# Kernel optimization log

Measured on AMD Instinct MI355X. Metric: run time of the kernel, lower is better.

## Reference

```python
import jax, jax.numpy as jnp
import numpy as np

B, A, F = 8192, 8, 256      # batch, n_agents, per-agent obs feature dim
NA = 16                     # n_actions per agent
H1, H2 = 1024, 1024
OBS_D = A * F               # 2048 flattened obs dim
ACT_D = A * NA              # 128 joint action dim
IN_D = OBS_D + ACT_D        # 2176 MLP input dim


def setup_inputs() -> dict:
    key = jax.random.key(0)
    ks = jax.random.split(key, 8)
    s = 0.02
    return {
        "obs": jax.random.normal(ks[0], (B, A, F), dtype=jnp.float32),
        "all_actions": jax.random.uniform(ks[1], (B, ACT_D), dtype=jnp.float32),
        # per-agent stacked MLP params (agent axis first)
        "W1": jax.random.normal(ks[2], (A, IN_D, H1), dtype=jnp.float32) * s,
        "b1": jnp.zeros((A, H1), dtype=jnp.float32),
        "W2": jax.random.normal(ks[3], (A, H1, H2), dtype=jnp.float32) * s,
        "b2": jnp.zeros((A, H2), dtype=jnp.float32),
        "W3": jax.random.normal(ks[4], (A, H2, NA), dtype=jnp.float32) * s,
        "b3": jnp.zeros((A, NA), dtype=jnp.float32),
    }


def reference(obs, all_actions, W1, b1, W2, b2, W3, b3):
    b_s = obs.shape[0]
    obs_flat = obs.reshape(b_s, OBS_D)                      # [B, A*F]
    # mask[a, g] = 0 on agent a's own action block, 1 elsewhere
    mask = 1.0 - jnp.repeat(jnp.eye(A, dtype=obs.dtype), NA, axis=1)  # [A, A*NA]
    # split W1 into obs / action columns (equivalent to concat-then-dense)
    W1o = W1[:, :OBS_D, :]                                  # [A, OBS_D, H1]
    W1a = W1[:, OBS_D:, :]                                  # [A, ACT_D, H1]
    h1 = jax.nn.relu(
        jnp.einsum("bd,adh->bah", obs_flat, W1o)
        + jnp.einsum("bg,ag,agh->bah", all_actions, mask, W1a)
        + b1
    )                                                        # [B, A, H1]
    h2 = jax.nn.relu(jnp.einsum("bah,ahk->bak", h1, W2) + b2)  # [B, A, H2]
    out = jnp.einsum("bak,akn->ban", h2, W3) + b3              # [B, A, NA]
    return out.reshape(b_s, A * NA)
```

## Files before the change

### kernel.cpp

```cpp
#include <hip/hip_runtime.h>
#include <hip/hip_bf16.h>
#include <cstdint>
#include <cstddef>

typedef __bf16 bf16;
typedef __attribute__((ext_vector_type(8))) __bf16 bf16x8;
typedef __attribute__((ext_vector_type(4))) float f32x4;
typedef __attribute__((ext_vector_type(4))) int i32x4;
typedef __attribute__((address_space(3))) const bf16* lds_cp;

#define B_SZ  8192
#define NAGENT 8
#define NA_N  16
#define OBS_DD 2048
#define ACT_DD 128
#define IN_DD 2176
#define H1_D  1024
#define H2_D  1024

#define BM 256
#define BN 256
#define BK 64
#define GRID_M (B_SZ / BM)
#define GRID_N (1024 / BN)

__device__ __forceinline__ void gload16(const void* g, void* l) {
    __builtin_amdgcn_global_load_lds(
        (__attribute__((address_space(1))) void*)(g),
        (__attribute__((address_space(3))) void*)(l), 16, 0, 0);
}

__global__ void k_prep(const float* __restrict__ obs, const float* __restrict__ act,
                       bf16* __restrict__ xb, const float* __restrict__ b3,
                       float* __restrict__ out, const float* __restrict__ W3,
                       bf16* __restrict__ w3t) {
    const int NX = B_SZ * (IN_DD / 8);
    const int NO = B_SZ * 128 / 4;
    const int NW3 = NAGENT * NA_N * H2_D;
    int idx = blockIdx.x * blockDim.x + threadIdx.x;
    if (idx < NX) {
        const int chunks = IN_DD / 8;
        int b = idx / chunks;
        int c8 = idx - b * chunks;
        const float* src = (c8 < OBS_DD / 8)
            ? (obs + (size_t)b * OBS_DD + c8 * 8)
            : (act + (size_t)b * ACT_DD + (c8 - OBS_DD / 8) * 8);
        float4 v0 = ((const float4*)src)[0];
        float4 v1 = ((const float4*)src)[1];
        bf16x8 o;
        o[0] = (bf16)v0.x; o[1] = (bf16)v0.y; o[2] = (bf16)v0.z; o[3] = (bf16)v0.w;
        o[4] = (bf16)v1.x; o[5] = (bf16)v1.y; o[6] = (bf16)v1.z; o[7] = (bf16)v1.w;
        ((bf16x8*)(xb + (size_t)b * IN_DD))[c8] = o;
    } else if (idx < NX + NO) {
        int i = idx - NX;
        int c = (i & 31) * 4;
        float4 v = make_float4(b3[c], b3[c + 1], b3[c + 2], b3[c + 3]);
        ((float4*)out)[i] = v;
    } else if (idx < NX + NO + NW3) {
        int i = idx - NX - NO;
        int a = i / (NA_N * H2_D);
        int n = (i / H2_D) % NA_N;
        int k = i % H2_D;
        w3t[i] = (bf16)W3[(size_t)a * H2_D * NAGENT * 0 + (size_t)a * H2_D * NA_N + (size_t)k * NA_N + n];
    }
}

__global__ void k_transpose_w12(const float* __restrict__ W1, bf16* __restrict__ W1T,
                                const float* __restrict__ W2, bf16* __restrict__ W2T) {
    __shared__ float tile[32][33];
    const int z = blockIdx.z;
    const bool isW1 = (z < 8);
    const int a = isW1 ? z : z - 8;
    const int K = isW1 ? IN_DD : H1_D;
    const int H = 1024;
    const int maskStart = isW1 ? OBS_DD : (1 << 30);
    if (!isW1 && blockIdx.x >= (H1_D / 32)) return;
    const float* s = (isW1 ? W1 : W2) + (size_t)a * K * H;
    bf16* d = (isW1 ? W1T : W2T) + (size_t)a * K * H;
    int k0 = blockIdx.x * 32, h0 = blockIdx.y * 32;
    int tx = threadIdx.x, ty = threadIdx.y;
    #pragma unroll
    for (int i = 0; i < 32; i += 8) {
        int k = k0 + ty + i;
        float v = s[(size_t)k * H + h0 + tx];
        if (k >= maskStart) {
            int g = k - maskStart;
            if ((g >> 4) == a) v = 0.f;
        }
        tile[ty + i][tx] = v;
    }
    __syncthreads();
    #pragma unroll
    for (int i = 0; i < 32; i += 8) {
        d[(size_t)(h0 + ty + i) * K + k0 + tx] = (bf16)tile[tx][ty + i];
    }
}

#define DSR4(d0, d1, d2, d3, addr, O0, O1, O2, O3)                      \
    asm volatile("ds_read_b128 %0, %4 offset:" #O0 "\n\t"               \
                 "ds_read_b128 %1, %4 offset:" #O1 "\n\t"               \
                 "ds_read_b128 %2, %4 offset:" #O2 "\n\t"               \
                 "ds_read_b128 %3, %4 offset:" #O3                      \
                 : "=&v"(d0), "=&v"(d1), "=&v"(d2), "=&v"(d3)           \
                 : "v"(addr))

#define BC(x) __builtin_bit_cast(bf16x8, x)

template<int FUSE>
__global__ __launch_bounds__(512, 1)
void k_gemm256(const bf16* __restrict__ Ain, size_t aStride, int lda,
               const bf16* __restrict__ Bw, const float* __restrict__ bias,
               bf16* __restrict__ Cout, size_t cStride, int K,
               int aOff, int gridZ,
               const bf16* __restrict__ W3Tp, float* __restrict__ outp) {
    extern __shared__ bf16 lds[];

    const int tid = threadIdx.x;
    const int w = tid >> 6;
    const int l = tid & 63;

    int flat = blockIdx.x + GRID_M * (blockIdx.y + GRID_N * blockIdx.z);
    int q8 = (GRID_M * GRID_N * gridZ) >> 3;
    int lin2 = (flat & 7) * q8 + (flat >> 3);
    const int mt = lin2 % GRID_M;
    int rest = lin2 / GRID_M;
    const int ntile = rest % GRID_N;
    const int az = rest / GRID_N;
    const int aw = az + aOff;

    const int rowBase = mt * BM;
    const int colBase = ntile * BN;
    const bf16* Aag = Ain + (size_t)az * aStride;
    const bf16* Bag = Bw + (size_t)aw * (size_t)1024 * K;

    const int wr = (w >> 2) * 128;
    const int wc = (w & 3) * 64;
    const int lr = l & 15;
    const int lq = l >> 4;

    const int rowA = (wr + lr) * BK;
    const int rowB = (wc + lr) * BK;
    const int ck0 = ((lq ^ (lr & 7)) * 8);
    const int ck1 = (((4 + lq) ^ (lr & 7)) * 8);

    const int sRow = w * 16 + (l >> 3);
    const int sCol = ((l & 7) ^ (l >> 3)) * 8;
    const bf16* pA0 = Aag + (size_t)(rowBase + sRow) * lda + sCol;
    const bf16* pA1 = Aag + (size_t)(rowBase + 128 + sRow) * lda + sCol;
    const bf16* pB0 = Bag + (size_t)(colBase + sRow) * K + sCol;
    const bf16* pB1 = Bag + (size_t)(colBase + 128 + sRow) * K + sCol;
    const size_t l8a = (size_t)8 * lda;
    const size_t l8b = (size_t)8 * K;

    const int nkt = K / BK;

#define STAGE_A(t1, half) do {                                              \
        const bf16* g_ = ((half) ? pA1 : pA0) + (t1) * BK;                  \
        bf16* d_ = &lds[(((t1) & 1) * 16384) + (half) * 8192 + w * 1024];   \
        gload16(g_, d_);                                                    \
        gload16(g_ + l8a, d_ + 512);                                        \
    } while (0)
#define STAGE_B(t2, half) do {                                              \
        const bf16* g_ = ((half) ? pB1 : pB0) + (t2) * BK;                  \
        bf16* d_ = &lds[32768 + (((t2) & 1) * 16384) + (half) * 8192 + w * 1024]; \
        gload16(g_, d_);                                                    \
        gload16(g_ + l8b, d_ + 512);                                        \
    } while (0)

    f32x4 acc[8][4] = {};
    i32x4 ra0, ra1, ra2, ra3;
    i32x4 rb0, rb1, rb2, rb3;
    i32x4 rc0, rc1, rc2, rc3;
    i32x4 rd0, rd1, rd2, rd3;
    i32x4 re0, re1, re2, re3;
    i32x4 rf0, rf1, rf2, rf3;

#define MFMA16(ACC0, A0, A1, A2, A3, B0, B1, B2, B3)                        \
    do {                                                                    \
        acc[ACC0+0][0] = __builtin_amdgcn_mfma_f32_16x16x32_bf16(BC(A0), BC(B0), acc[ACC0+0][0], 0, 0, 0); \
        acc[ACC0+1][0] = __builtin_amdgcn_mfma_f32_16x16x32_bf16(BC(A1), BC(B0), acc[ACC0+1][0], 0, 0, 0); \
        acc[ACC0+2][0] = __builtin_amdgcn_mfma_f32_16x16x32_bf16(BC(A2), BC(B0), acc[ACC0+2][0], 0, 0, 0); \
        acc[ACC0+3][0] = __builtin_amdgcn_mfma_f32_16x16x32_bf16(BC(A3), BC(B0), acc[ACC0+3][0], 0, 0, 0); \
        acc[ACC0+0][1] = __builtin_amdgcn_mfma_f32_16x16x32_bf16(BC(A0), BC(B1), acc[ACC0+0][1], 0, 0, 0); \
        acc[ACC0+1][1] = __builtin_amdgcn_mfma_f32_16x16x32_bf16(BC(A1), BC(B1), acc[ACC0+1][1], 0, 0, 0); \
        acc[ACC0+2][1] = __builtin_amdgcn_mfma_f32_16x16x32_bf16(BC(A2), BC(B1), acc[ACC0+2][1], 0, 0, 0); \
        acc[ACC0+3][1] = __builtin_amdgcn_mfma_f32_16x16x32_bf16(BC(A3), BC(B1), acc[ACC0+3][1], 0, 0, 0); \
        acc[ACC0+0][2] = __builtin_amdgcn_mfma_f32_16x16x32_bf16(BC(A0), BC(B2), acc[ACC0+0][2], 0, 0, 0); \
        acc[ACC0+1][2] = __builtin_amdgcn_mfma_f32_16x16x32_bf16(BC(A1), BC(B2), acc[ACC0+1][2], 0, 0, 0); \
        acc[ACC0+2][2] = __builtin_amdgcn_mfma_f32_16x16x32_bf16(BC(A2), BC(B2), acc[ACC0+2][2], 0, 0, 0); \
        acc[ACC0+3][2] = __builtin_amdgcn_mfma_f32_16x16x32_bf16(BC(A3), BC(B2), acc[ACC0+3][2], 0, 0, 0); \
        acc[ACC0+0][3] = __builtin_amdgcn_mfma_f32_16x16x32_bf16(BC(A0), BC(B3), acc[ACC0+0][3], 0, 0, 0); \
        acc[ACC0+1][3] = __builtin_amdgcn_mfma_f32_16x16x32_bf16(BC(A1), BC(B3), acc[ACC0+1][3], 0, 0, 0); \
        acc[ACC0+2][3] = __builtin_amdgcn_mfma_f32_16x16x32_bf16(BC(A2), BC(B3), acc[ACC0+2][3], 0, 0, 0); \
        acc[ACC0+3][3] = __builtin_amdgcn_mfma_f32_16x16x32_bf16(BC(A3), BC(B3), acc[ACC0+3][3], 0, 0, 0); \
    } while (0)

    STAGE_A(0, 0); STAGE_A(0, 1);
    STAGE_B(0, 0); STAGE_B(0, 1);
    asm volatile("s_waitcnt vmcnt(0)" ::: "memory");
    __builtin_amdgcn_s_barrier();

    for (int t = 0; t < nkt; ++t) {
        const int dbuf = (t & 1) * 16384;
        lds_cp adrA0 = (lds_cp)lds + (dbuf + rowA + ck0);
        lds_cp adrA1 = (lds_cp)lds + (dbuf + rowA + ck1);
        lds_cp adrB0 = (lds_cp)lds + (32768 + dbuf + rowB + ck0);
        lds_cp adrB1 = (lds_cp)lds + (32768 + dbuf + rowB + ck1);

        DSR4(ra0, ra1, ra2, ra3, adrA0, 0, 2048, 4096, 6144);
        DSR4(rb0, rb1, rb2, rb3, adrB0, 0, 2048, 4096, 6144);
        DSR4(rc0, rc1, rc2, rc3, adrA0, 8192, 10240, 12288, 14336);
        DSR4(rd0, rd1, rd2, rd3, adrB1, 0, 2048, 4096, 6144);

        if (t + 1 < nkt) {
            STAGE_A(t + 1, 0); STAGE_A(t + 1, 1);
            STAGE_B(t + 1, 0); STAGE_B(t + 1, 1);
        }

        asm volatile("s_waitcnt lgkmcnt(8)" ::: "memory");
        __builtin_amdgcn_sched_barrier(0);
        __builtin_amdgcn_s_setprio(1);
        MFMA16(0, ra0, ra1, ra2, ra3, rb0, rb1, rb2, rb3);
        __builtin_amdgcn_s_setprio(0);

        DSR4(re0, re1, re2, re3, adrA1, 0, 2048, 4096, 6144);
        asm volatile("s_waitcnt lgkmcnt(4)" ::: "memory");
        __builtin_amdgcn_sched_barrier(0);
        __builtin_amdgcn_s_setprio(1);
        MFMA16(4, rc0, rc1, rc2, rc3, rb0, rb1, rb2, rb3);
        __builtin_amdgcn_s_setprio(0);

        DSR4(rf0, rf1, rf2, rf3, adrA1, 8192, 10240, 12288, 14336);
        asm volatile("s_waitcnt lgkmcnt(4)" ::: "memory");
        __builtin_amdgcn_sched_barrier(0);
        __builtin_amdgcn_s_setprio(1);
        MFMA16(0, re0, re1, re2, re3, rd0, rd1, rd2, rd3);
        __builtin_amdgcn_s_setprio(0);

        asm volatile("s_waitcnt vmcnt(0)" ::: "memory");
        asm volatile("s_waitcnt lgkmcnt(0)" ::: "memory");
        __builtin_amdgcn_sched_barrier(0);
        __builtin_amdgcn_s_setprio(1);
        MFMA16(4, rf0, rf1, rf2, rf3, rd0, rd1, rd2, rd3);
        __builtin_amdgcn_s_setprio(0);

        __builtin_amdgcn_s_barrier();
    }
#undef STAGE_A
#undef STAGE_B
#undef MFMA16

    __syncthreads();
    const float* bAg = bias + (size_t)aw * 1024;
    float bb4[4];
    #pragma unroll
    for (int n = 0; n < 4; ++n) bb4[n] = bAg[colBase + wc + n * 16 + lr];
    #pragma unroll
    for (int m = 0; m < 8; ++m)
        #pragma unroll
        for (int n = 0; n < 4; ++n)
            #pragma unroll
            for (int r = 0; r < 4; ++r) {
                float v = acc[m][n][r] + bb4[n];
                v = fmaxf(v, 0.f);
                int row = wr + m * 16 + lq * 4 + r;
                int col = wc + n * 16 + lr;
                lds[row * 256 + ((((col >> 3) ^ (row & 7)) << 3) | (col & 7))] = (bf16)v;
            }
    __syncthreads();

    if constexpr (!FUSE) {
        bf16* Cg = Cout + (size_t)az * cStride + (size_t)rowBase * 1024 + colBase;
        const int er = tid >> 5;
        const int ec = tid & 31;
        #pragma unroll
        for (int i = 0; i < 16; ++i) {
            int row = i * 16 + er;
            int phys = ec ^ (row & 7);
            *(bf16x8*)&Cg[(size_t)row * 1024 + ec * 8] =
                *(const bf16x8*)&lds[row * 256 + phys * 8];
        }
    } else {
        const bf16* w3a = W3Tp + (size_t)aw * NA_N * H2_D;
        f32x4 oacc[2] = {};
        const int frow0 = w * 32;
        #pragma unroll
        for (int ks = 0; ks < 8; ++ks) {
            bf16x8 bfrag = *(const bf16x8*)&w3a[(size_t)lr * H2_D + colBase + ks * 32 + lq * 8];
            #pragma unroll
            for (int mm = 0; mm < 2; ++mm) {
                int row = frow0 + mm * 16 + lr;
                int lc = (ks * 4 + lq) ^ (row & 7);
                bf16x8 afrag = *(const bf16x8*)&lds[row * 256 + lc * 8];
                oacc[mm] = __builtin_amdgcn_mfma_f32_16x16x32_bf16(afrag, bfrag, oacc[mm], 0, 0, 0);
            }
        }
        #pragma unroll
        for (int mm = 0; mm < 2; ++mm)
            #pragma unroll
            for (int r = 0; r < 4; ++r)
                atomicAdd(&outp[(size_t)(rowBase + frow0 + mm * 16 + lq * 4 + r) * 128
                                + aw * NA_N + lr], oacc[mm][r]);
    }
}

extern "C" void kernel_launch(void* const* d_in, const int* in_sizes, int n_in,
                              void* d_out, int out_size, void* d_ws, size_t ws_size,
                              hipStream_t stream) {
    const float* obs = (const float*)d_in[0];
    const float* act = (const float*)d_in[1];
    const float* W1 = (const float*)d_in[2];
    const float* b1 = (const float*)d_in[3];
    const float* W2 = (const float*)d_in[4];
    const float* b2 = (const float*)d_in[5];
    const float* W3 = (const float*)d_in[6];
    const float* b3 = (const float*)d_in[7];
    float* out = (float*)d_out;

    const size_t SZ_XB  = (size_t)B_SZ * IN_DD * 2;
    const size_t SZ_W1T = (size_t)NAGENT * H1_D * IN_DD * 2;
    const size_t SZ_W2T = (size_t)NAGENT * H1_D * H2_D * 2;
    const size_t SZ_W3T = (size_t)NAGENT * NA_N * H2_D * 2;
    const size_t SZ_H1  = (size_t)B_SZ * H1_D * 2;
    const size_t SZ_FIX = SZ_XB + SZ_W1T + SZ_W2T + SZ_W3T;

    char* ws = (char*)d_ws;
    bf16* Xb  = (bf16*)ws;
    bf16* W1T = (bf16*)(ws + SZ_XB);
    bf16* W2T = (bf16*)(ws + SZ_XB + SZ_W1T);
    bf16* W3T = (bf16*)(ws + SZ_XB + SZ_W1T + SZ_W2T);
    char* hbase = ws + SZ_FIX;

    int G = 8;
    while (G > 1 && ws_size < SZ_FIX + (size_t)G * SZ_H1) G >>= 1;

    (void)hipFuncSetAttribute((const void*)k_gemm256<0>,
                              hipFuncAttributeMaxDynamicSharedMemorySize, 131072);
    (void)hipFuncSetAttribute((const void*)k_gemm256<1>,
                              hipFuncAttributeMaxDynamicSharedMemorySize, 131072);

    {
        const int NX = B_SZ * (IN_DD / 8);
        const int NO = B_SZ * 128 / 4;
        const int NW3 = NAGENT * NA_N * H2_D;
        int n = NX + NO + NW3;
        k_prep<<<(n + 255) / 256, 256, 0, stream>>>(obs, act, Xb, b3, out, W3, W3T);
    }
    k_transpose_w12<<<dim3(IN_DD / 32, 1024 / 32, 16), dim3(32, 8), 0, stream>>>(
        W1, W1T, W2, W2T);

    const size_t agElems = (size_t)B_SZ * H1_D;
    bf16* h1 = (bf16*)hbase;

    for (int g0 = 0; g0 < NAGENT; g0 += G) {
        k_gemm256<0><<<dim3(GRID_M, GRID_N, G), 512, 131072, stream>>>(
            Xb, 0, IN_DD, W1T, b1, h1, agElems, IN_DD, g0, G, nullptr, nullptr);
        k_gemm256<1><<<dim3(GRID_M, GRID_N, G), 512, 131072, stream>>>(
            h1, agElems, H1_D, W2T, b2, nullptr, 0, H1_D, g0, G, W3T, out);
    }
    (void)in_sizes; (void)n_in; (void)out_size;
}
```

Baseline: 441.9 us.

## Restructure GEMM inner loop into row-pair MFMA clusters and reorder tile raster

The main loop now keeps all eight B fragments resident and streams A fragments in pairs of row tiles, with double-buffered A registers (pa/qa) interleaved with four MFMA clusters. This replaces the old scheme of four 16-MFMA groups each fed by separate A/B loads. The goal is finer-grained overlap of LDS reads with MFMA and lower register pressure for A. The block raster order also changes so N tiles vary fastest, which changes which blocks share A rows in L2. A redundant zero term in the W3 transpose index is removed.

```diff
diff --git a/kernel.cpp b/kernel.cpp
--- a/kernel.cpp
+++ b/kernel.cpp
@@ -61,7 +61,7 @@
         int a = i / (NA_N * H2_D);
         int n = (i / H2_D) % NA_N;
         int k = i % H2_D;
-        w3t[i] = (bf16)W3[(size_t)a * H2_D * NAGENT * 0 + (size_t)a * H2_D * NA_N + (size_t)k * NA_N + n];
+        w3t[i] = (bf16)W3[(size_t)a * H2_D * NA_N + (size_t)k * NA_N + n];
     }
 }
 
@@ -103,6 +103,10 @@
                  "ds_read_b128 %3, %4 offset:" #O3                      \
                  : "=&v"(d0), "=&v"(d1), "=&v"(d2), "=&v"(d3)           \
                  : "v"(addr))
+#define DSR2(d0, d1, addr, O0, O1)                                      \
+    asm volatile("ds_read_b128 %0, %2 offset:" #O0 "\n\t"               \
+                 "ds_read_b128 %1, %2 offset:" #O1                      \
+                 : "=&v"(d0), "=&v"(d1) : "v"(addr))
 
 #define BC(x) __builtin_bit_cast(bf16x8, x)
 
@@ -122,10 +126,10 @@
     int flat = blockIdx.x + GRID_M * (blockIdx.y + GRID_N * blockIdx.z);
     int q8 = (GRID_M * GRID_N * gridZ) >> 3;
     int lin2 = (flat & 7) * q8 + (flat >> 3);
-    const int mt = lin2 % GRID_M;
-    int rest = lin2 / GRID_M;
-    const int ntile = rest % GRID_N;
-    const int az = rest / GRID_N;
+    const int ntile = lin2 % GRID_N;
+    int rest = lin2 / GRID_N;
+    const int mt = rest % GRID_M;
+    const int az = rest / GRID_M;
     const int aw = az + aOff;
 
     const int rowBase = mt * BM;
@@ -168,31 +172,28 @@
     } while (0)
 
     f32x4 acc[8][4] = {};
-    i32x4 ra0, ra1, ra2, ra3;
-    i32x4 rb0, rb1, rb2, rb3;
-    i32x4 rc0, rc1, rc2, rc3;
-    i32x4 rd0, rd1, rd2, rd3;
-    i32x4 re0, re1, re2, re3;
-    i32x4 rf0, rf1, rf2, rf3;
-
-#define MFMA16(ACC0, A0, A1, A2, A3, B0, B1, B2, B3)                        \
+    i32x4 rb0, rb1, rb2, rb3, rb4, rb5, rb6, rb7;
+    i32x4 pa0, pa1, pa2, pa3;
+    i32x4 qa0, qa1, qa2, qa3;
+
+#define CLUST(M0, a0, a1, a2, a3)                                           \
     do {                                                                    \
-        acc[ACC0+0][0] = __builtin_amdgcn_mfma_f32_16x16x32_bf16(BC(A0), BC(B0), acc[ACC0+0][0], 0, 0, 0); \
-        acc[ACC0+1][0] = __builtin_amdgcn_mfma_f32_16x16x32_bf16(BC(A1), BC(B0), acc[ACC0+1][0], 0, 0, 0); \
-        acc[ACC0+2][0] = __builtin_amdgcn_mfma_f32_16x16x32_bf16(BC(A2), BC(B0), acc[ACC0+2][0], 0, 0, 0); \
-        acc[ACC0+3][0] = __builtin_amdgcn_mfma_f32_16x16x32_bf16(BC(A3), BC(B0), acc[ACC0+3][0], 0, 0, 0); \
-        acc[ACC0+0][1] = __builtin_amdgcn_mfma_f32_16x16x32_bf16(BC(A0), BC(B1), acc[ACC0+0][1], 0, 0, 0); \
-        acc[ACC0+1][1] = __builtin_amdgcn_mfma_f32_16x16x32_bf16(BC(A1), BC(B1), acc[ACC0+1][1], 0, 0, 0); \
-        acc[ACC0+2][1] = __builtin_amdgcn_mfma_f32_16x16x32_bf16(BC(A2), BC(B1), acc[ACC0+2][1], 0, 0, 0); \
-        acc[ACC0+3][1] = __builtin_amdgcn_mfma_f32_16x16x32_bf16(BC(A3), BC(B1), acc[ACC0+3][1], 0, 0, 0); \
-        acc[ACC0+0][2] = __builtin_amdgcn_mfma_f32_16x16x32_bf16(BC(A0), BC(B2), acc[ACC0+0][2], 0, 0, 0); \
-        acc[ACC0+1][2] = __builtin_amdgcn_mfma_f32_16x16x32_bf16(BC(A1), BC(B2), acc[ACC0+1][2], 0, 0, 0); \
-        acc[ACC0+2][2] = __builtin_amdgcn_mfma_f32_16x16x32_bf16(BC(A2), BC(B2), acc[ACC0+2][2], 0, 0, 0); \
-        acc[ACC0+3][2] = __builtin_amdgcn_mfma_f32_16x16x32_bf16(BC(A3), BC(B2), acc[ACC0+3][2], 0, 0, 0); \
-        acc[ACC0+0][3] = __builtin_amdgcn_mfma_f32_16x16x32_bf16(BC(A0), BC(B3), acc[ACC0+0][3], 0, 0, 0); \
-        acc[ACC0+1][3] = __builtin_amdgcn_mfma_f32_16x16x32_bf16(BC(A1), BC(B3), acc[ACC0+1][3], 0, 0, 0); \
-        acc[ACC0+2][3] = __builtin_amdgcn_mfma_f32_16x16x32_bf16(BC(A2), BC(B3), acc[ACC0+2][3], 0, 0, 0); \
-        acc[ACC0+3][3] = __builtin_amdgcn_mfma_f32_16x16x32_bf16(BC(A3), BC(B3), acc[ACC0+3][3], 0, 0, 0); \
+        acc[M0+0][0] = __builtin_amdgcn_mfma_f32_16x16x32_bf16(BC(a0), BC(rb0), acc[M0+0][0], 0, 0, 0); \
+        acc[M0+1][0] = __builtin_amdgcn_mfma_f32_16x16x32_bf16(BC(a1), BC(rb0), acc[M0+1][0], 0, 0, 0); \
+        acc[M0+0][1] = __builtin_amdgcn_mfma_f32_16x16x32_bf16(BC(a0), BC(rb1), acc[M0+0][1], 0, 0, 0); \
+        acc[M0+1][1] = __builtin_amdgcn_mfma_f32_16x16x32_bf16(BC(a1), BC(rb1), acc[M0+1][1], 0, 0, 0); \
+        acc[M0+0][2] = __builtin_amdgcn_mfma_f32_16x16x32_bf16(BC(a0), BC(rb2), acc[M0+0][2], 0, 0, 0); \
+        acc[M0+1][2] = __builtin_amdgcn_mfma_f32_16x16x32_bf16(BC(a1), BC(rb2), acc[M0+1][2], 0, 0, 0); \
+        acc[M0+0][3] = __builtin_amdgcn_mfma_f32_16x16x32_bf16(BC(a0), BC(rb3), acc[M0+0][3], 0, 0, 0); \
+        acc[M0+1][3] = __builtin_amdgcn_mfma_f32_16x16x32_bf16(BC(a1), BC(rb3), acc[M0+1][3], 0, 0, 0); \
+        acc[M0+0][0] = __builtin_amdgcn_mfma_f32_16x16x32_bf16(BC(a2), BC(rb4), acc[M0+0][0], 0, 0, 0); \
+        acc[M0+1][0] = __builtin_amdgcn_mfma_f32_16x16x32_bf16(BC(a3), BC(rb4), acc[M0+1][0], 0, 0, 0); \
+        acc[M0+0][1] = __builtin_amdgcn_mfma_f32_16x16x32_bf16(BC(a2), BC(rb5), acc[M0+0][1], 0, 0, 0); \
+        acc[M0+1][1] = __builtin_amdgcn_mfma_f32_16x16x32_bf16(BC(a3), BC(rb5), acc[M0+1][1], 0, 0, 0); \
+        acc[M0+0][2] = __builtin_amdgcn_mfma_f32_16x16x32_bf16(BC(a2), BC(rb6), acc[M0+0][2], 0, 0, 0); \
+        acc[M0+1][2] = __builtin_amdgcn_mfma_f32_16x16x32_bf16(BC(a3), BC(rb6), acc[M0+1][2], 0, 0, 0); \
+        acc[M0+0][3] = __builtin_amdgcn_mfma_f32_16x16x32_bf16(BC(a2), BC(rb7), acc[M0+0][3], 0, 0, 0); \
+        acc[M0+1][3] = __builtin_amdgcn_mfma_f32_16x16x32_bf16(BC(a3), BC(rb7), acc[M0+1][3], 0, 0, 0); \
     } while (0)
 
     STAGE_A(0, 0); STAGE_A(0, 1);
@@ -207,48 +208,55 @@
         lds_cp adrB0 = (lds_cp)lds + (32768 + dbuf + rowB + ck0);
         lds_cp adrB1 = (lds_cp)lds + (32768 + dbuf + rowB + ck1);
 
-        DSR4(ra0, ra1, ra2, ra3, adrA0, 0, 2048, 4096, 6144);
+        DSR2(pa0, pa1, adrA0, 0, 2048);
+        DSR2(pa2, pa3, adrA1, 0, 2048);
         DSR4(rb0, rb1, rb2, rb3, adrB0, 0, 2048, 4096, 6144);
-        DSR4(rc0, rc1, rc2, rc3, adrA0, 8192, 10240, 12288, 14336);
-        DSR4(rd0, rd1, rd2, rd3, adrB1, 0, 2048, 4096, 6144);
+        DSR4(rb4, rb5, rb6, rb7, adrB1, 0, 2048, 4096, 6144);
 
         if (t + 1 < nkt) {
             STAGE_A(t + 1, 0); STAGE_A(t + 1, 1);
             STAGE_B(t + 1, 0); STAGE_B(t + 1, 1);
         }
 
-        asm volatile("s_waitcnt lgkmcnt(8)" ::: "memory");
-        __builtin_amdgcn_sched_barrier(0);
-        __builtin_amdgcn_s_setprio(1);
-        MFMA16(0, ra0, ra1, ra2, ra3, rb0, rb1, rb2, rb3);
-        __builtin_amdgcn_s_setprio(0);
-
-        DSR4(re0, re1, re2, re3, adrA1, 0, 2048, 4096, 6144);
+        DSR2(qa0, qa1, adrA0, 4096, 6144);
+        DSR2(qa2, qa3, adrA1, 4096, 6144);
+
         asm volatile("s_waitcnt lgkmcnt(4)" ::: "memory");
         __builtin_amdgcn_sched_barrier(0);
         __builtin_amdgcn_s_setprio(1);
-        MFMA16(4, rc0, rc1, rc2, rc3, rb0, rb1, rb2, rb3);
+        CLUST(0, pa0, pa1, pa2, pa3);
         __builtin_amdgcn_s_setprio(0);
 
-        DSR4(rf0, rf1, rf2, rf3, adrA1, 8192, 10240, 12288, 14336);
+        DSR2(pa0, pa1, adrA0, 8192, 10240);
+        DSR2(pa2, pa3, adrA1, 8192, 10240);
+
         asm volatile("s_waitcnt lgkmcnt(4)" ::: "memory");
         __builtin_amdgcn_sched_barrier(0);
         __builtin_amdgcn_s_setprio(1);
-        MFMA16(0, re0, re1, re2, re3, rd0, rd1, rd2, rd3);
+        CLUST(2, qa0, qa1, qa2, qa3);
+        __builtin_amdgcn_s_setprio(0);
+
+        DSR2(qa0, qa1, adrA0, 12288, 14336);
+        DSR2(qa2, qa3, adrA1, 12288, 14336);
+
+        asm volatile("s_waitcnt lgkmcnt(4)" ::: "memory");
+        __builtin_amdgcn_sched_barrier(0);
+        __builtin_amdgcn_s_setprio(1);
+        CLUST(4, pa0, pa1, pa2, pa3);
         __builtin_amdgcn_s_setprio(0);
 
         asm volatile("s_waitcnt vmcnt(0)" ::: "memory");
         asm volatile("s_waitcnt lgkmcnt(0)" ::: "memory");
         __builtin_amdgcn_sched_barrier(0);
         __builtin_amdgcn_s_setprio(1);
-        MFMA16(4, rf0, rf1, rf2, rf3, rd0, rd1, rd2, rd3);
+        CLUST(6, qa0, qa1, qa2, qa3);
         __builtin_amdgcn_s_setprio(0);
 
         __builtin_amdgcn_s_barrier();
     }
 #undef STAGE_A
 #undef STAGE_B
-#undef MFMA16
+#undef CLUST
 
     __syncthreads();
     const float* bAg = bias + (size_t)aw * 1024;
```

Measured after the change: 418.7 us. 1.06x faster.
